# Kernel tuning notes

Hardware: AMD Instinct MI355X
Metric: run time of the kernel (lower is better)

## Reference

```python
import jax, jax.numpy as jnp
import numpy as np

B, H, W, C = 4, 64, 64, 64
GROUPS = 32
EPS = 1e-3  # keras GroupNormalization default


def setup_inputs() -> dict:
    key = jax.random.key(0)
    ks = jax.random.split(key, 6)
    s = 1.0 / np.sqrt(C)
    return {
        'x': jax.random.normal(ks[0], (B, H, W, C), dtype=jnp.float32),
        'gamma': jnp.ones((C,), jnp.float32),
        'beta': jnp.zeros((C,), jnp.float32),
        'wq': jax.random.uniform(ks[1], (C, C), jnp.float32, -s, s),
        'bq': jnp.zeros((C,), jnp.float32),
        'wk': jax.random.uniform(ks[2], (C, C), jnp.float32, -s, s),
        'bk': jnp.zeros((C,), jnp.float32),
        'wv': jax.random.uniform(ks[3], (C, C), jnp.float32, -s, s),
        'bv': jnp.zeros((C,), jnp.float32),
        'wo': jnp.zeros((C, C), jnp.float32),  # init_scale=0.0 -> ~zero init
        'bo': jnp.zeros((C,), jnp.float32),
    }


def group_norm(x, gamma, beta):
    b, h, w, c = x.shape
    xg = x.reshape(b, h, w, GROUPS, c // GROUPS)
    mean = jnp.mean(xg, axis=(1, 2, 4), keepdims=True)
    var = jnp.var(xg, axis=(1, 2, 4), keepdims=True)
    xn = ((xg - mean) * jax.lax.rsqrt(var + EPS)).reshape(b, h, w, c)
    return xn * gamma + beta


def reference(x, gamma, beta, wq, bq, wk, bk, wv, bv, wo, bo):
    b, h, w, c = x.shape
    hn = group_norm(x, gamma, beta)
    # 1x1 convs == per-pixel dense layers
    q = jnp.einsum('bhwc,cd->bhwd', hn, wq) + bq
    k = jnp.einsum('bhwc,cd->bhwd', hn, wk) + bk
    v = jnp.einsum('bhwc,cd->bhwd', hn, wv) + bv
    # full spatial attention scores [B,H,W,H,W]
    scores = jnp.einsum('bhwc,bHWc->bhwHW', q, k) * (float(c) ** -0.5)
    attn = jax.nn.softmax(scores.reshape(b, h, w, h * w), axis=-1)
    attn = attn.reshape(b, h, w, h, w)
    o = jnp.einsum('bhwHW,bHWc->bhwc', attn, v)
    o = jnp.einsum('bhwc,cd->bhwd', o, wo) + bo
    return x + o
```

## Files before the change

### kernel.cpp

```cpp
#include <hip/hip_runtime.h>
#include <math.h>

#define BB 4
#define HH 64
#define WW 64
#define CC 64
#define NN (HH*WW)
#define NPIX (BB*NN)
#define EPS 1e-3f
#define QBLK 32
#define KSPLIT 8
#define NQT32 (NPIX/QBLK)
#define NCHK ((NN/KSPLIT)/64)

using bf16x8 = __attribute__((ext_vector_type(8))) short;
using f32x4  = __attribute__((ext_vector_type(4))) float;
using f32x16 = __attribute__((ext_vector_type(16))) float;

__device__ inline unsigned short bf16bits(float f) {
    union { float f; unsigned u; } a; a.f = f;
    unsigned r = a.u + 0x7fffu + ((a.u >> 16) & 1u);
    return (unsigned short)(r >> 16);
}
__device__ inline unsigned packbf(float lo, float hi) {
    return (unsigned)bf16bits(lo) | ((unsigned)bf16bits(hi) << 16);
}
__device__ inline unsigned cvtpk(float lo, float hi) {
    unsigned r;
    asm("v_cvt_pk_bf16_f32 %0, %1, %2" : "=v"(r) : "v"(lo), "v"(hi));
    return r;
}
#define PSWAP(a, b) asm("v_permlane32_swap_b32 %0, %1" : "+v"(a), "+v"(b))

__device__ __forceinline__ float exp2g(float x) {
    float r;
    asm("v_exp_f32 %0, %1" : "=v"(r) : "v"(x));
    return r;
}

#define QSCALE 0.18033688011112042f

__global__ __launch_bounds__(256) void gn_wt(const float* __restrict__ x,
                                             float* __restrict__ part,
                                             const float* __restrict__ wq,
                                             const float* __restrict__ wk,
                                             const float* __restrict__ wv,
                                             const float* __restrict__ wo,
                                             short* __restrict__ wfrag) {
    int t = threadIdx.x;
    if (blockIdx.x < 256) {
        int c = t & 63, rr = t >> 6;
        int p0 = blockIdx.x * 64;
        float s = 0.f, s2 = 0.f;
        #pragma unroll
        for (int k = 0; k < 16; ++k) {
            float v = x[(size_t)(p0 + rr + 4 * k) * CC + c];
            s += v; s2 += v * v;
        }
        __shared__ float sA[256], sB[256];
        sA[t] = s; sB[t] = s2;
        __syncthreads();
        if (t < 64) {
            float fs  = sA[t] + sA[64 + t] + sA[128 + t] + sA[192 + t];
            float fs2 = sB[t] + sB[64 + t] + sB[128 + t] + sB[192 + t];
            part[blockIdx.x * 128 + t]      = fs;
            part[blockIdx.x * 128 + 64 + t] = fs2;
        }
    } else {
        const float* mats[3] = {wq, wk, wv};
        int i0 = (blockIdx.x - 256) * 256 + t;
        for (int e = i0; e < 12288; e += 16 * 256) {
            int m = e >> 12;
            int r = e & 4095;
            int dt = r >> 10, h = (r >> 9) & 1, lane = (r >> 3) & 63, j = r & 7;
            int g = lane >> 4, cl = lane & 15;
            float v = mats[m][(h * 32 + g * 8 + j) * 64 + dt * 16 + cl];
            wfrag[e] = (short)bf16bits(v);
        }
        for (int e = i0; e < 4096; e += 16 * 256) {
            int j = e & 7, lane = (e >> 3) & 63, dt = (e >> 9) & 1, s = e >> 10;
            int hi = lane >> 5, l31 = lane & 31;
            float v = wo[(8 * hi + 16 * s + j) * 64 + dt * 32 + l31];
            wfrag[12288 + e] = (short)bf16bits(v);
        }
    }
}

__global__ __launch_bounds__(256) void qkv_proj(
        const float* __restrict__ x,
        const float* __restrict__ part,
        const float* __restrict__ gamma,
        const float* __restrict__ beta,
        const short* __restrict__ wfrag,
        const float* __restrict__ bq, const float* __restrict__ bk,
        const float* __restrict__ bv,
        short* __restrict__ qb, short* __restrict__ kb,
        short* __restrict__ vt) {
    __shared__ unsigned short vtile[64 * 72];
    __shared__ float sA[256], sB[256];
    __shared__ float sScale[64], sShift[64];
    int t = threadIdx.x;
    int lane = t & 63, wid = t >> 6;
    int g = lane >> 4, cl = lane & 15;
    int pixblk = blockIdx.x * 64;
    int pix0 = pixblk + wid * 16;
    int b = pixblk >> 12;

    {
        int c = t & 63, rr = t >> 6;
        float s = 0.f, s2 = 0.f;
        #pragma unroll
        for (int k = 0; k < 16; ++k) {
            int blk = b * 64 + rr + 4 * k;
            s  += part[blk * 128 + c];
            s2 += part[blk * 128 + 64 + c];
        }
        sA[t] = s; sB[t] = s2;
        __syncthreads();
        if (t < 64) {
            sA[t] = sA[t] + sA[64 + t] + sA[128 + t] + sA[192 + t];
            sB[t] = sB[t] + sB[64 + t] + sB[128 + t] + sB[192 + t];
        }
        __syncthreads();
        if (t < 64) {
            int gg = t >> 1;
            float sumg  = sA[gg * 2] + sA[gg * 2 + 1];
            float sum2g = sB[gg * 2] + sB[gg * 2 + 1];
            const float n = (float)(NN * 2);
            float mean = sumg / n;
            float var  = sum2g / n - mean * mean;
            float r = rsqrtf(var + EPS);
            float a = gamma[t] * r;
            sScale[t] = a;
            sShift[t] = beta[t] - mean * a;
        }
        __syncthreads();
    }

    const float* xp = x + (size_t)(pix0 + cl) * CC + g * 8;
    float4 x00 = *(const float4*)(xp);
    float4 x01 = *(const float4*)(xp + 4);
    float4 x10 = *(const float4*)(xp + 32);
    float4 x11 = *(const float4*)(xp + 36);
    float4 s00 = *(const float4*)(&sScale[g * 8]);
    float4 s01 = *(const float4*)(&sScale[g * 8 + 4]);
    float4 s10 = *(const float4*)(&sScale[g * 8 + 32]);
    float4 s11 = *(const float4*)(&sScale[g * 8 + 36]);
    float4 f00 = *(const float4*)(&sShift[g * 8]);
    float4 f01 = *(const float4*)(&sShift[g * 8 + 4]);
    float4 f10 = *(const float4*)(&sShift[g * 8 + 32]);
    float4 f11 = *(const float4*)(&sShift[g * 8 + 36]);

    union { bf16x8 v; unsigned u[4]; } af0, af1;
    af0.u[0] = packbf(x00.x * s00.x + f00.x, x00.y * s00.y + f00.y);
    af0.u[1] = packbf(x00.z * s00.z + f00.z, x00.w * s00.w + f00.w);
    af0.u[2] = packbf(x01.x * s01.x + f01.x, x01.y * s01.y + f01.y);
    af0.u[3] = packbf(x01.z * s01.z + f01.z, x01.w * s01.w + f01.w);
    af1.u[0] = packbf(x10.x * s10.x + f10.x, x10.y * s10.y + f10.y);
    af1.u[1] = packbf(x10.z * s10.z + f10.z, x10.w * s10.w + f10.w);
    af1.u[2] = packbf(x11.x * s11.x + f11.x, x11.y * s11.y + f11.y);
    af1.u[3] = packbf(x11.z * s11.z + f11.z, x11.w * s11.w + f11.w);

    #pragma unroll
    for (int m = 0; m < 3; ++m) {
        const float* bias = (m == 0) ? bq : (m == 1) ? bk : bv;
        #pragma unroll
        for (int dt = 0; dt < 4; ++dt) {
            bf16x8 w0 = *(const bf16x8*)(wfrag + (size_t)(((m * 4 + dt) * 2 + 0) * 64 + lane) * 8);
            bf16x8 w1 = *(const bf16x8*)(wfrag + (size_t)(((m * 4 + dt) * 2 + 1) * 64 + lane) * 8);
            f32x4 z = (f32x4){0.f, 0.f, 0.f, 0.f};
            z = __builtin_amdgcn_mfma_f32_16x16x32_bf16(af0.v, w0, z, 0, 0, 0);
            z = __builtin_amdgcn_mfma_f32_16x16x32_bf16(af1.v, w1, z, 0, 0, 0);
            float bias_d = bias[dt * 16 + cl];
            if (m == 0) {
                #pragma unroll
                for (int r = 0; r < 4; ++r)
                    qb[(size_t)(pix0 + 4 * g + r) * CC + dt * 16 + cl] =
                        (short)bf16bits((z[r] + bias_d) * QSCALE);
            } else if (m == 1) {
                #pragma unroll
                for (int r = 0; r < 4; ++r)
                    kb[(size_t)(pix0 + 4 * g + r) * CC + dt * 16 + cl] =
                        (short)bf16bits(z[r] + bias_d);
            } else {
                #pragma unroll
                for (int r = 0; r < 4; ++r)
                    vtile[(dt * 16 + cl) * 72 + wid * 16 + 4 * g + r] =
                        bf16bits(z[r] + bias_d);
            }
        }
    }
    __syncthreads();
    {
        int d = t >> 2, seg = t & 3;
        uint4 v0 = *(const uint4*)(vtile + d * 72 + seg * 16);
        uint4 v1 = *(const uint4*)(vtile + d * 72 + seg * 16 + 8);
        uint4* dst = (uint4*)(vt + ((size_t)(b * 64 + d)) * NN + pixblk + seg * 16);
        dst[0] = v0; dst[1] = v1;
    }
}

__global__ __launch_bounds__(512, 4) void attn_flash(
        const short* __restrict__ qb, const short* __restrict__ kb,
        const short* __restrict__ vt,
        unsigned* __restrict__ obf, float* __restrict__ msb) {
    __shared__ short lds[3][2][64 * 64];
    const int t = threadIdx.x;
    const int lane = t & 63;
    const int wid  = t >> 6;
    const int hi  = lane >> 5;
    const int l31 = lane & 31;
    const int r7  = l31 & 7;
    const int kseg   = blockIdx.x % KSPLIT;
    const int qblock = blockIdx.x / KSPLIT;
    const int qtile  = qblock * 8 + wid;
    const int b = qblock >> 4;
    const int key0 = kseg * (NN / KSPLIT);

    bf16x8 qf[4];
    const short* qp = qb + (size_t)(qtile * QBLK + l31) * CC + 8 * hi;
    #pragma unroll
    for (int s = 0; s < 4; ++s) qf[s] = *(const bf16x8*)(qp + 16 * s);

    const int srow = t >> 3;
    const int scol = t & 7;
    const short* kS = kb + ((size_t)b * NN + key0) * CC;
    const short* vS = vt + ((size_t)b * CC) * NN + key0;

    f32x16 oacc0, oacc1;
    #pragma unroll
    for (int r = 0; r < 16; ++r) { oacc0[r] = 0.f; oacc1[r] = 0.f; }
    float psum = 0.f;

    auto stage = [&](int ck, int bsel) {
        const short* srcK = kS + (size_t)(ck * 64 + srow) * CC + (scol ^ (srow & 7)) * 8;
        __builtin_amdgcn_global_load_lds(
            (const __attribute__((address_space(1))) void*)srcK,
            (__attribute__((address_space(3))) void*)&lds[bsel][0][wid * 512],
            16, 0, 0);
        const short* srcV = vS + (size_t)srow * NN + ck * 64 + (scol ^ (srow & 7)) * 8;
        __builtin_amdgcn_global_load_lds(
            (const __attribute__((address_space(1))) void*)srcV,
            (__attribute__((address_space(3))) void*)&lds[bsel][1][wid * 512],
            16, 0, 0);
    };

    auto subbody = [&](const short* kB, const short* vB, int ks) {
        bf16x8 kf[4];
        #pragma unroll
        for (int s = 0; s < 4; ++s)
            kf[s] = *(const bf16x8*)(kB + (32 * ks + l31) * 64 + ((2 * s + hi) ^ r7) * 8);
        bf16x8 vf0 = *(const bf16x8*)(vB + (l31) * 64      + ((4 * ks + 0 + hi) ^ r7) * 8);
        bf16x8 vf1 = *(const bf16x8*)(vB + (32 + l31) * 64 + ((4 * ks + 0 + hi) ^ r7) * 8);
        bf16x8 vf2 = *(const bf16x8*)(vB + (l31) * 64      + ((4 * ks + 2 + hi) ^ r7) * 8);
        bf16x8 vf3 = *(const bf16x8*)(vB + (32 + l31) * 64 + ((4 * ks + 2 + hi) ^ r7) * 8);
        f32x16 st;
        #pragma unroll
        for (int r = 0; r < 16; ++r) st[r] = 0.f;
        #pragma unroll
        for (int s = 0; s < 4; ++s)
            st = __builtin_amdgcn_mfma_f32_32x32x16_bf16(kf[s], qf[s], st, 0, 0, 0);
        float ps = 0.f;
        #pragma unroll
        for (int r = 0; r < 16; ++r) { st[r] = exp2g(st[r]); ps += st[r]; }
        psum += ps;
        unsigned w[8];
        #pragma unroll
        for (int i = 0; i < 8; ++i) w[i] = cvtpk(st[2 * i], st[2 * i + 1]);
        PSWAP(w[0], w[2]); PSWAP(w[1], w[3]);
        PSWAP(w[4], w[6]); PSWAP(w[5], w[7]);
        union { bf16x8 v; unsigned u[4]; } pa0, pa1;
        pa0.u[0] = w[0]; pa0.u[1] = w[1]; pa0.u[2] = w[2]; pa0.u[3] = w[3];
        pa1.u[0] = w[4]; pa1.u[1] = w[5]; pa1.u[2] = w[6]; pa1.u[3] = w[7];
        oacc0 = __builtin_amdgcn_mfma_f32_32x32x16_bf16(pa0.v, vf0, oacc0, 0, 0, 0);
        oacc1 = __builtin_amdgcn_mfma_f32_32x32x16_bf16(pa0.v, vf1, oacc1, 0, 0, 0);
        oacc0 = __builtin_amdgcn_mfma_f32_32x32x16_bf16(pa1.v, vf2, oacc0, 0, 0, 0);
        oacc1 = __builtin_amdgcn_mfma_f32_32x32x16_bf16(pa1.v, vf3, oacc1, 0, 0, 0);
    };

    stage(0, 0);
    stage(1, 1);
    #pragma unroll 1
    for (int c = 0; c < NCHK - 1; ++c) {
        asm volatile("s_waitcnt vmcnt(2)" ::: "memory");
        __builtin_amdgcn_s_barrier();
        if (c + 2 < NCHK) stage(c + 2, (c + 2) % 3);
        const short* kB = &lds[c % 3][0][0];
        const short* vB = &lds[c % 3][1][0];
        subbody(kB, vB, 0);
        subbody(kB, vB, 1);
    }
    asm volatile("s_waitcnt vmcnt(0)" ::: "memory");
    __builtin_amdgcn_s_barrier();
    {
        const int c = NCHK - 1;
        const short* kB = &lds[c % 3][0][0];
        const short* vB = &lds[c % 3][1][0];
        subbody(kB, vB, 0);
        subbody(kB, vB, 1);
    }

    int task = qtile * KSPLIT + kseg;
    unsigned* ob32 = obf + (size_t)task * 1024;
    #pragma unroll
    for (int r = 0; r < 16; ++r) {
        int row = (r & 3) + 8 * (r >> 2) + 4 * hi;
        ob32[row * 32 + l31] = cvtpk(oacc0[r], oacc1[r]);
    }
    msb[task * 64 + lane] = psum;
}

__device__ __forceinline__ void acc2(float& lo_acc, float& hi_acc, unsigned u) {
    union { unsigned u; float f; } a, b;
    a.u = u << 16; b.u = u & 0xffff0000u;
    lo_acc += a.f; hi_acc += b.f;
}

__global__ __launch_bounds__(256) void attn_merge_outproj(
        const unsigned* __restrict__ obf, const float* __restrict__ msb,
        const short* __restrict__ wfrag,
        const float* __restrict__ x,
        const float* __restrict__ bo,
        float* __restrict__ out) {
    int t = threadIdx.x;
    int lane = t & 63, wid = t >> 6;
    int hi = lane >> 5, l31 = lane & 31;
    int qtile = blockIdx.x * 4 + wid;

    float stot = 0.f;
    #pragma unroll
    for (int s = 0; s < KSPLIT; ++s) {
        stot += msb[(qtile * KSPLIT + s) * 64 + l31]
              + msb[(qtile * KSPLIT + s) * 64 + 32 + l31];
    }
    float inv = 1.f / stot;

    float oa[4][8];
    #pragma unroll
    for (int s = 0; s < 4; ++s)
        #pragma unroll
        for (int j = 0; j < 8; ++j) oa[s][j] = 0.f;
    #pragma unroll 4
    for (int ks = 0; ks < KSPLIT; ++ks) {
        const unsigned* base = obf + (size_t)(qtile * KSPLIT + ks) * 1024 + l31 * 32 + 8 * hi;
        uint4 wa = *(const uint4*)(base);
        uint4 wb = *(const uint4*)(base + 4);
        uint4 wc = *(const uint4*)(base + 16);
        uint4 wd = *(const uint4*)(base + 20);
        acc2(oa[0][0], oa[2][0], wa.x); acc2(oa[0][1], oa[2][1], wa.y);
        acc2(oa[0][2], oa[2][2], wa.z); acc2(oa[0][3], oa[2][3], wa.w);
        acc2(oa[0][4], oa[2][4], wb.x); acc2(oa[0][5], oa[2][5], wb.y);
        acc2(oa[0][6], oa[2][6], wb.z); acc2(oa[0][7], oa[2][7], wb.w);
        acc2(oa[1][0], oa[3][0], wc.x); acc2(oa[1][1], oa[3][1], wc.y);
        acc2(oa[1][2], oa[3][2], wc.z); acc2(oa[1][3], oa[3][3], wc.w);
        acc2(oa[1][4], oa[3][4], wd.x); acc2(oa[1][5], oa[3][5], wd.y);
        acc2(oa[1][6], oa[3][6], wd.z); acc2(oa[1][7], oa[3][7], wd.w);
    }
    union { bf16x8 v; unsigned u[4]; } af[4];
    #pragma unroll
    for (int s = 0; s < 4; ++s)
        #pragma unroll
        for (int m = 0; m < 4; ++m)
            af[s].u[m] = cvtpk(oa[s][2 * m] * inv, oa[s][2 * m + 1] * inv);

    const short* w32 = wfrag + 12288;
    f32x16 z0, z1;
    #pragma unroll
    for (int r = 0; r < 16; ++r) { z0[r] = 0.f; z1[r] = 0.f; }
    #pragma unroll
    for (int s = 0; s < 4; ++s) {
        bf16x8 wb0 = *(const bf16x8*)(w32 + (size_t)((s * 2 + 0) * 64 + lane) * 8);
        bf16x8 wb1 = *(const bf16x8*)(w32 + (size_t)((s * 2 + 1) * 64 + lane) * 8);
        z0 = __builtin_amdgcn_mfma_f32_32x32x16_bf16(af[s].v, wb0, z0, 0, 0, 0);
        z1 = __builtin_amdgcn_mfma_f32_32x32x16_bf16(af[s].v, wb1, z1, 0, 0, 0);
    }
    float bo0 = bo[l31], bo1 = bo[32 + l31];
    #pragma unroll
    for (int r = 0; r < 16; ++r) {
        int row = (r & 3) + 8 * (r >> 2) + 4 * hi;
        size_t i0 = (size_t)(qtile * QBLK + row) * CC + l31;
        out[i0]      = x[i0]      + z0[r] + bo0;
        out[i0 + 32] = x[i0 + 32] + z1[r] + bo1;
    }
}

extern "C" void kernel_launch(void* const* d_in, const int* in_sizes, int n_in,
                              void* d_out, int out_size, void* d_ws, size_t ws_size,
                              hipStream_t stream) {
    const float* x     = (const float*)d_in[0];
    const float* gamma = (const float*)d_in[1];
    const float* beta  = (const float*)d_in[2];
    const float* wq    = (const float*)d_in[3];
    const float* bq    = (const float*)d_in[4];
    const float* wk    = (const float*)d_in[5];
    const float* bk    = (const float*)d_in[6];
    const float* wv    = (const float*)d_in[7];
    const float* bv    = (const float*)d_in[8];
    const float* wo    = (const float*)d_in[9];
    const float* bo    = (const float*)d_in[10];
    float* out = (float*)d_out;

    float* ws    = (float*)d_ws;
    float* part  = ws;
    short* wfrag = (short*)(part + 32768);
    short* qb    = wfrag + 16384;
    short* kbp   = qb  + (size_t)NPIX * CC;
    short* vtp   = kbp + (size_t)NPIX * CC;
    unsigned* obf = (unsigned*)(vtp + (size_t)NPIX * CC);
    float* msb   = (float*)(obf + (size_t)NQT32 * KSPLIT * 1024);

    hipLaunchKernelGGL(gn_wt, dim3(272), dim3(256), 0, stream,
                       x, part, wq, wk, wv, wo, wfrag);
    hipLaunchKernelGGL(qkv_proj, dim3(256), dim3(256), 0, stream,
                       x, part, gamma, beta, wfrag, bq, bk, bv, qb, kbp, vtp);
    hipLaunchKernelGGL(attn_flash, dim3(64 * KSPLIT), dim3(512), 0, stream,
                       qb, kbp, vtp, obf, msb);
    hipLaunchKernelGGL(attn_merge_outproj, dim3(NQT32 / 4), dim3(256), 0, stream,
                       obf, msb, wfrag, x, bo, out);
}
```

Before: 45.60 us.

## Apply output projection per KV split inside flash kernel, simplify merge to elementwise

The output projection is moved into the end of the attention kernel. Each split's unnormalized partial output is transposed through LDS into MFMA A-fragments and multiplied by Wo there, which is valid because the projection is linear. The final kernel then only sums the projected partials, divides by the softmax denominator, and adds the residual and bias in a simple elementwise pass. The trade is more MFMA work, since the projection runs once per KV split (8x) rather than once per query tile, plus an extra LDS round trip and barrier in the flash epilogue. In return the merge kernel becomes a simpler, more parallel elementwise pass.

```diff
diff --git a/kernel.cpp b/kernel.cpp
--- a/kernel.cpp
+++ b/kernel.cpp
@@ -202,7 +202,7 @@
 
 __global__ __launch_bounds__(512, 4) void attn_flash(
         const short* __restrict__ qb, const short* __restrict__ kb,
-        const short* __restrict__ vt,
+        const short* __restrict__ vt, const short* __restrict__ wfrag,
         unsigned* __restrict__ obf, float* __restrict__ msb) {
     __shared__ short lds[3][2][64 * 64];
     const int t = threadIdx.x;
@@ -300,88 +300,70 @@
         subbody(kB, vB, 1);
     }
 
+    __syncthreads();
+    unsigned* scr = (unsigned*)&lds[0][0][0] + (size_t)wid * (32 * 36);
+    #pragma unroll
+    for (int r = 0; r < 16; ++r) {
+        int row = (r & 3) + 8 * (r >> 2) + 4 * hi;
+        scr[row * 36 + l31] = cvtpk(oacc0[r], oacc1[r]);
+    }
+    uint4 wa0 = *(const uint4*)(scr + l31 * 36 + 8 * hi);
+    uint4 wa1 = *(const uint4*)(scr + l31 * 36 + 8 * hi + 4);
+    uint4 wb0_ = *(const uint4*)(scr + l31 * 36 + 16 + 8 * hi);
+    uint4 wb1_ = *(const uint4*)(scr + l31 * 36 + 16 + 8 * hi + 4);
+    unsigned wA[8] = {wa0.x, wa0.y, wa0.z, wa0.w, wa1.x, wa1.y, wa1.z, wa1.w};
+    unsigned wB[8] = {wb0_.x, wb0_.y, wb0_.z, wb0_.w, wb1_.x, wb1_.y, wb1_.z, wb1_.w};
+    union { bf16x8 v; unsigned u[4]; } af[4];
+    #pragma unroll
+    for (int m = 0; m < 4; ++m) {
+        af[0].u[m] = (wA[2 * m] & 0xffffu) | (wA[2 * m + 1] << 16);
+        af[1].u[m] = (wB[2 * m] & 0xffffu) | (wB[2 * m + 1] << 16);
+        af[2].u[m] = (wA[2 * m] >> 16) | (wA[2 * m + 1] & 0xffff0000u);
+        af[3].u[m] = (wB[2 * m] >> 16) | (wB[2 * m + 1] & 0xffff0000u);
+    }
+    const short* w32 = wfrag + 12288;
+    f32x16 z0, z1;
+    #pragma unroll
+    for (int r = 0; r < 16; ++r) { z0[r] = 0.f; z1[r] = 0.f; }
+    #pragma unroll
+    for (int s = 0; s < 4; ++s) {
+        bf16x8 wo0 = *(const bf16x8*)(w32 + (size_t)((s * 2 + 0) * 64 + lane) * 8);
+        bf16x8 wo1 = *(const bf16x8*)(w32 + (size_t)((s * 2 + 1) * 64 + lane) * 8);
+        z0 = __builtin_amdgcn_mfma_f32_32x32x16_bf16(af[s].v, wo0, z0, 0, 0, 0);
+        z1 = __builtin_amdgcn_mfma_f32_32x32x16_bf16(af[s].v, wo1, z1, 0, 0, 0);
+    }
     int task = qtile * KSPLIT + kseg;
     unsigned* ob32 = obf + (size_t)task * 1024;
     #pragma unroll
     for (int r = 0; r < 16; ++r) {
         int row = (r & 3) + 8 * (r >> 2) + 4 * hi;
-        ob32[row * 32 + l31] = cvtpk(oacc0[r], oacc1[r]);
+        ob32[row * 32 + l31] = cvtpk(z0[r], z1[r]);
     }
     msb[task * 64 + lane] = psum;
 }
 
-__device__ __forceinline__ void acc2(float& lo_acc, float& hi_acc, unsigned u) {
-    union { unsigned u; float f; } a, b;
-    a.u = u << 16; b.u = u & 0xffff0000u;
-    lo_acc += a.f; hi_acc += b.f;
-}
-
-__global__ __launch_bounds__(256) void attn_merge_outproj(
+__global__ __launch_bounds__(256) void merge_ew(
         const unsigned* __restrict__ obf, const float* __restrict__ msb,
-        const short* __restrict__ wfrag,
-        const float* __restrict__ x,
-        const float* __restrict__ bo,
+        const float* __restrict__ x, const float* __restrict__ bo,
         float* __restrict__ out) {
-    int t = threadIdx.x;
-    int lane = t & 63, wid = t >> 6;
-    int hi = lane >> 5, l31 = lane & 31;
-    int qtile = blockIdx.x * 4 + wid;
-
-    float stot = 0.f;
+    int u = blockIdx.x * 256 + threadIdx.x;
+    int q = u >> 5, c31 = u & 31;
+    int qtile = q >> 5;
+    int zbase = (qtile * KSPLIT) * 1024 + (q & 31) * 32 + c31;
+    int mbase = (qtile * KSPLIT) * 64 + (q & 31);
+    float zlo = 0.f, zhi = 0.f, ssum = 0.f;
     #pragma unroll
     for (int s = 0; s < KSPLIT; ++s) {
-        stot += msb[(qtile * KSPLIT + s) * 64 + l31]
-              + msb[(qtile * KSPLIT + s) * 64 + 32 + l31];
-    }
-    float inv = 1.f / stot;
-
-    float oa[4][8];
-    #pragma unroll
-    for (int s = 0; s < 4; ++s)
-        #pragma unroll
-        for (int j = 0; j < 8; ++j) oa[s][j] = 0.f;
-    #pragma unroll 4
-    for (int ks = 0; ks < KSPLIT; ++ks) {
-        const unsigned* base = obf + (size_t)(qtile * KSPLIT + ks) * 1024 + l31 * 32 + 8 * hi;
-        uint4 wa = *(const uint4*)(base);
-        uint4 wb = *(const uint4*)(base + 4);
-        uint4 wc = *(const uint4*)(base + 16);
-        uint4 wd = *(const uint4*)(base + 20);
-        acc2(oa[0][0], oa[2][0], wa.x); acc2(oa[0][1], oa[2][1], wa.y);
-        acc2(oa[0][2], oa[2][2], wa.z); acc2(oa[0][3], oa[2][3], wa.w);
-        acc2(oa[0][4], oa[2][4], wb.x); acc2(oa[0][5], oa[2][5], wb.y);
-        acc2(oa[0][6], oa[2][6], wb.z); acc2(oa[0][7], oa[2][7], wb.w);
-        acc2(oa[1][0], oa[3][0], wc.x); acc2(oa[1][1], oa[3][1], wc.y);
-        acc2(oa[1][2], oa[3][2], wc.z); acc2(oa[1][3], oa[3][3], wc.w);
-        acc2(oa[1][4], oa[3][4], wd.x); acc2(oa[1][5], oa[3][5], wd.y);
-        acc2(oa[1][6], oa[3][6], wd.z); acc2(oa[1][7], oa[3][7], wd.w);
-    }
-    union { bf16x8 v; unsigned u[4]; } af[4];
-    #pragma unroll
-    for (int s = 0; s < 4; ++s)
-        #pragma unroll
-        for (int m = 0; m < 4; ++m)
-            af[s].u[m] = cvtpk(oa[s][2 * m] * inv, oa[s][2 * m + 1] * inv);
-
-    const short* w32 = wfrag + 12288;
-    f32x16 z0, z1;
-    #pragma unroll
-    for (int r = 0; r < 16; ++r) { z0[r] = 0.f; z1[r] = 0.f; }
-    #pragma unroll
-    for (int s = 0; s < 4; ++s) {
-        bf16x8 wb0 = *(const bf16x8*)(w32 + (size_t)((s * 2 + 0) * 64 + lane) * 8);
-        bf16x8 wb1 = *(const bf16x8*)(w32 + (size_t)((s * 2 + 1) * 64 + lane) * 8);
-        z0 = __builtin_amdgcn_mfma_f32_32x32x16_bf16(af[s].v, wb0, z0, 0, 0, 0);
-        z1 = __builtin_amdgcn_mfma_f32_32x32x16_bf16(af[s].v, wb1, z1, 0, 0, 0);
-    }
-    float bo0 = bo[l31], bo1 = bo[32 + l31];
-    #pragma unroll
-    for (int r = 0; r < 16; ++r) {
-        int row = (r & 3) + 8 * (r >> 2) + 4 * hi;
-        size_t i0 = (size_t)(qtile * QBLK + row) * CC + l31;
-        out[i0]      = x[i0]      + z0[r] + bo0;
-        out[i0 + 32] = x[i0 + 32] + z1[r] + bo1;
-    }
+        unsigned w = obf[zbase + s * 1024];
+        union { unsigned u; float f; } a, b2;
+        a.u = w << 16; b2.u = w & 0xffff0000u;
+        zlo += a.f; zhi += b2.f;
+        ssum += msb[mbase + s * 64] + msb[mbase + s * 64 + 32];
+    }
+    float inv = 1.f / ssum;
+    size_t i0 = (size_t)q * CC + c31;
+    out[i0]      = x[i0]      + bo[c31]      + zlo * inv;
+    out[i0 + 32] = x[i0 + 32] + bo[c31 + 32] + zhi * inv;
 }
 
 extern "C" void kernel_launch(void* const* d_in, const int* in_sizes, int n_in,
@@ -414,7 +396,7 @@
     hipLaunchKernelGGL(qkv_proj, dim3(256), dim3(256), 0, stream,
                        x, part, gamma, beta, wfrag, bq, bk, bv, qb, kbp, vtp);
     hipLaunchKernelGGL(attn_flash, dim3(64 * KSPLIT), dim3(512), 0, stream,
-                       qb, kbp, vtp, obf, msb);
-    hipLaunchKernelGGL(attn_merge_outproj, dim3(NQT32 / 4), dim3(256), 0, stream,
-                       obf, msb, wfrag, x, bo, out);
-}
+                       qb, kbp, vtp, wfrag, obf, msb);
+    hipLaunchKernelGGL(merge_ew, dim3(2048), dim3(256), 0, stream,
+                       obf, msb, x, bo, out);
+}
```

Result: no change. 45.05 us (-1.2%).
